# Kernel optimization log

Measured on AMD Instinct MI355X. Metric: run time of the kernel, lower is better.

## Reference

```python
import jax, jax.numpy as jnp
import numpy as np

D_MODEL = 1024
N_HEADS = 16
D_KV = 64
INNER = N_HEADS * D_KV
NUM_BUCKETS = 32
MAX_DISTANCE = 128
B, S = 4, 2048


def _relative_position_bucket(relative_position):
    # Mirrors T5Attention._relative_position_bucket (bidirectional variant)
    num_buckets = NUM_BUCKETS // 2  # 16
    relative_buckets = (relative_position > 0).astype(jnp.int32) * num_buckets
    rp = jnp.abs(relative_position)
    max_exact = num_buckets // 2  # 8
    is_small = rp < max_exact
    # clamp to 1 before log to avoid -inf (masked out by where anyway)
    rp_large = max_exact + (
        jnp.log(jnp.maximum(rp, 1).astype(jnp.float32) / max_exact)
        / np.log(MAX_DISTANCE / max_exact)
        * (num_buckets - max_exact)
    ).astype(jnp.int32)
    rp_large = jnp.minimum(rp_large, num_buckets - 1)
    return relative_buckets + jnp.where(is_small, rp.astype(jnp.int32), rp_large)


def setup_inputs() -> dict:
    key = jax.random.key(0)
    k1, k2, k3, k4, k5, k6 = jax.random.split(key, 6)
    hidden_states = jax.random.normal(k1, (B, S, D_MODEL), dtype=jnp.float32)
    positions = jnp.arange(B * S, dtype=jnp.int64 if jax.config.jax_enable_x64 else jnp.int32).reshape(B, S)
    mask = jnp.ones((B, S), dtype=jnp.float32)
    sc = 1.0 / np.sqrt(D_MODEL)
    wq = jax.random.normal(k2, (INNER, D_MODEL), dtype=jnp.float32) * sc
    wk = jax.random.normal(k3, (INNER, D_MODEL), dtype=jnp.float32) * sc
    wv = jax.random.normal(k4, (INNER, D_MODEL), dtype=jnp.float32) * sc
    wo = jax.random.normal(k5, (D_MODEL, INNER), dtype=jnp.float32) * sc
    rel_bias = jax.random.normal(k6, (NUM_BUCKETS, N_HEADS), dtype=jnp.float32)
    return {"hidden_states": hidden_states, "positions": positions, "mask": mask,
            "wq": wq, "wk": wk, "wv": wv, "wo": wo, "rel_bias": rel_bias}


def reference(hidden_states, positions, mask, wq, wk, wv, wo, rel_bias):
    Bq, Sq, _ = hidden_states.shape

    def shape_heads(x):  # [B,S,inner] -> [B,H,S,dkv]
        return x.reshape(Bq, Sq, N_HEADS, D_KV).transpose(0, 2, 1, 3)

    # position bias: [B,H,Sq,Sk]
    rel_pos = positions[:, None, :] - positions[:, :, None]  # memory - context
    buckets = _relative_position_bucket(rel_pos)             # [B,Sq,Sk]
    position_bias = rel_bias[buckets].transpose(0, 3, 1, 2)  # [B,H,Sq,Sk]

    q = shape_heads(hidden_states @ wq.T).astype(jnp.float32)
    k = shape_heads(hidden_states @ wk.T).astype(jnp.float32)
    v = shape_heads(hidden_states @ wv.T).astype(jnp.float32)

    scores = jnp.einsum('bhqd,bhkd->bhqk', q, k)  # no 1/sqrt(d) scaling (T5)
    bias = position_bias - 1000.0 * (1.0 - mask[:, None, None, :])
    attn = jax.nn.softmax(scores + bias, axis=-1)  # dropout p=0

    ctx = jnp.einsum('bhqk,bhkd->bhqd', attn, v)
    ctx = ctx.transpose(0, 2, 1, 3).reshape(Bq, Sq, INNER).astype(hidden_states.dtype)
    return ctx @ wo.T
```

## Files before the change

kernel.cpp:

```cpp
#include <hip/hip_runtime.h>
#include <cstdint>
#include <cstddef>

#define D_MODEL 1024
#define N_HEADS 16
#define INNER   1024
#define NBATCH  4
#define SEQ     2048
#define MTOT    (NBATCH * SEQ)
#define LOG2E   1.44269504088896f
#define BSTRIDE 4352
#define MASKC   1442.695041f

typedef _Float16 f16;
typedef __attribute__((ext_vector_type(8))) _Float16 f16x8;
typedef __attribute__((ext_vector_type(4))) _Float16 f16x4;
typedef __attribute__((ext_vector_type(2))) _Float16 f16x2;
typedef __attribute__((ext_vector_type(2))) __fp16   h16x2;
typedef __attribute__((ext_vector_type(4))) float    f32x4;

__device__ __forceinline__ f16x2 cvtpk(float x, float y) {
#if __has_builtin(__builtin_amdgcn_cvt_pkrtz)
  h16x2 r = __builtin_amdgcn_cvt_pkrtz(x, y);
  return __builtin_bit_cast(f16x2, r);
#else
  f16x2 r; r[0] = (f16)x; r[1] = (f16)y; return r;
#endif
}
__device__ __forceinline__ float dot2acc(f16x2 p, float acc) {
#if __has_builtin(__builtin_amdgcn_fdot2)
  h16x2 a = __builtin_bit_cast(h16x2, p);
  h16x2 one; one[0] = (__fp16)1.0f; one[1] = (__fp16)1.0f;
  return __builtin_amdgcn_fdot2(a, one, acc, false);
#else
  return acc + (float)p[0] + (float)p[1];
#endif
}

__global__ void k_cvt(const float* __restrict__ src, f16* __restrict__ dst, int n4, float scale) {
  int i = blockIdx.x * 256 + threadIdx.x;
  if (i < n4) {
    const float4 v = reinterpret_cast<const float4*>(src)[i];
    f16x4 h;
    h[0] = (f16)(v.x * scale); h[1] = (f16)(v.y * scale);
    h[2] = (f16)(v.z * scale); h[3] = (f16)(v.w * scale);
    reinterpret_cast<f16x4*>(dst)[i] = h;
  }
}

__global__ void k_cvtw(const float* __restrict__ wq, const float* __restrict__ wk,
                       const float* __restrict__ wv, const float* __restrict__ wo,
                       f16* __restrict__ dq, f16* __restrict__ dk,
                       f16* __restrict__ dv, f16* __restrict__ dwo) {
  const int y = blockIdx.y;
  const float* src = y == 0 ? wq : (y == 1 ? wk : (y == 2 ? wv : wo));
  f16* dst = y == 0 ? dq : (y == 1 ? dk : (y == 2 ? dv : dwo));
  const float scale = y == 0 ? LOG2E : 1.0f;
  const int i = blockIdx.x * 256 + threadIdx.x;
  const float4 v = reinterpret_cast<const float4*>(src)[i];
  f16x4 h;
  h[0] = (f16)(v.x * scale); h[1] = (f16)(v.y * scale);
  h[2] = (f16)(v.z * scale); h[3] = (f16)(v.w * scale);
  reinterpret_cast<f16x4*>(dst)[i] = h;
}

__global__ void k_bias(const float* __restrict__ relb, float* __restrict__ biasG) {
  const int i = blockIdx.x * 256 + threadIdx.x;
  const int h = blockIdx.y;
  const int d = i - 2048;
  const int sgn = d > 0 ? 16 : 0;
  const int a = d < 0 ? -d : d;
  int bucket;
  if (a < 8) {
    bucket = a;
  } else {
    float t = logf((float)a / 8.0f);
    t = t / 2.772588722239781f;
    t = t * 8.0f;
    int lg = 8 + (int)t;
    bucket = lg < 15 ? lg : 15;
  }
  biasG[h * BSTRIDE + i] = relb[(sgn + bucket) * N_HEADS + h] * LOG2E - MASKC;
}

__device__ __forceinline__ void gload_lds16(const void* g, void* l) {
  __builtin_amdgcn_global_load_lds(
      (const __attribute__((address_space(1))) unsigned int*)g,
      (__attribute__((address_space(3))) unsigned int*)l,
      16, 0, 0);
}

template <int MODE>
__device__ __forceinline__ void gemm_body(const f16* __restrict__ A,
                                          const f16* __restrict__ W,
                                          void* __restrict__ Cp,
                                          int m0, int n0) {
  __shared__ __align__(16) f16 As[128 * 64];
  __shared__ __align__(16) f16 Bs[128 * 64];
  const int t = threadIdx.x;
  const int lane = t & 63;
  const int wid = t >> 6;
  const int wr = wid >> 1;
  const int wc = wid & 1;
  const int g = lane >> 4;
  const int lr = lane & 15;

  f32x4 acc[4][4] = {};
  const char* Ab = (const char*)A;
  const char* Wb = (const char*)W;

  for (int kt = 0; kt < D_MODEL / 64; ++kt) {
    const int k0 = kt * 64;
    __syncthreads();
#pragma unroll
    for (int i = 0; i < 4; ++i) {
      const int idx = i * 256 + t;
      const int row = idx >> 3;
      const int cb  = (idx & 7) * 16;
      gload_lds16(Ab + ((size_t)(m0 + row) * D_MODEL + k0) * 2 + cb, (char*)As + idx * 16);
      gload_lds16(Wb + ((size_t)(n0 + row) * D_MODEL + k0) * 2 + cb, (char*)Bs + idx * 16);
    }
    asm volatile("s_waitcnt vmcnt(0)" ::: "memory");
    __syncthreads();

    f16x8 af[4][2], bf[4][2];
#pragma unroll
    for (int mi = 0; mi < 4; ++mi)
#pragma unroll
      for (int kk = 0; kk < 2; ++kk)
        af[mi][kk] = *(const f16x8*)&As[(wr * 64 + mi * 16 + lr) * 64 + kk * 32 + g * 8];
#pragma unroll
    for (int ni = 0; ni < 4; ++ni)
#pragma unroll
      for (int kk = 0; kk < 2; ++kk)
        bf[ni][kk] = *(const f16x8*)&Bs[(wc * 64 + ni * 16 + lr) * 64 + kk * 32 + g * 8];
#pragma unroll
    for (int kk = 0; kk < 2; ++kk)
#pragma unroll
      for (int mi = 0; mi < 4; ++mi)
#pragma unroll
        for (int ni = 0; ni < 4; ++ni)
          acc[mi][ni] = __builtin_amdgcn_mfma_f32_16x16x32_f16(af[mi][kk], bf[ni][kk], acc[mi][ni], 0, 0, 0);
  }

#pragma unroll
  for (int mi = 0; mi < 4; ++mi)
#pragma unroll
    for (int ni = 0; ni < 4; ++ni) {
      const int n = n0 + wc * 64 + ni * 16 + lr;
      if (MODE == 2) {
        const int mbase = m0 + wr * 64 + mi * 16 + g * 4;
        const int b2 = mbase >> 11, s2 = mbase & (SEQ - 1);
        const int h2 = n >> 6, d2 = n & 63;
        const int sub = ((s2 & 15) >> 2) * 8 + ((s2 >> 4) & 1) * 4;
        f16x4 w;
#pragma unroll
        for (int r = 0; r < 4; ++r) w[r] = (f16)acc[mi][ni][r];
        *(f16x4*)((f16*)Cp + ((size_t)((b2 * 16 + h2) * 64 + d2) * SEQ + (s2 >> 5) * 32 + sub)) = w;
      } else {
#pragma unroll
        for (int r = 0; r < 4; ++r) {
          const int m = m0 + wr * 64 + mi * 16 + g * 4 + r;
          if (MODE == 1)
            ((float*)Cp)[(size_t)m * INNER + n] = acc[mi][ni][r];
          else
            ((f16*)Cp)[(size_t)m * INNER + n] = (f16)acc[mi][ni][r];
        }
      }
    }
}

__global__ __launch_bounds__(256) void k_gemm_qkv(
    const f16* __restrict__ A,
    const f16* __restrict__ Wq, const f16* __restrict__ Wk, const f16* __restrict__ Wv,
    f16* __restrict__ Cq, f16* __restrict__ Ck, f16* __restrict__ Vt) {
  const int bid = (int)blockIdx.x;
  const int X = bid & 7, l = bid >> 3;
  const int zy = X * 24 + (l >> 3);
  const int x = l & 7;
  const int z = zy >> 6, y = zy & 63;
  if (z == 0)      gemm_body<0>(A, Wq, Cq, y * 128, x * 128);
  else if (z == 1) gemm_body<0>(A, Wk, Ck, y * 128, x * 128);
  else             gemm_body<2>(A, Wv, Vt, y * 128, x * 128);
}

__global__ __launch_bounds__(256) void k_gemm_out(
    const f16* __restrict__ A, const f16* __restrict__ W, float* __restrict__ C) {
  const int bid = (int)blockIdx.x;
  const int X = bid & 7, l = bid >> 3;
  const int y = X * 8 + (l >> 3), x = l & 7;
  gemm_body<1>(A, W, C, y * 128, x * 128);
}

__global__ __launch_bounds__(512, 4) void k_attn(
    const f16* __restrict__ Q, const f16* __restrict__ K, const f16* __restrict__ Vt,
    const float* __restrict__ biasG, const float* __restrict__ mask,
    f16* __restrict__ ctx) {
  __shared__ __align__(16) float biasQ[4 * 2308];
  __shared__ __align__(16) f16 Ks[2 * 2048];
  __shared__ __align__(16) f16 Vs[2 * 2048];
  __shared__ int mflag;

  const int nb = (int)blockIdx.x;
  const int v = (nb & 7) * 64 + (nb >> 3);
  const int bh = v >> 3, qc = v & 7;
  const int b = bh >> 4, h = bh & 15;

  const int t = threadIdx.x, lane = t & 63, wid = t >> 6;
  const int g = lane >> 4, lr = lane & 15;
  const int qb = qc * 256;

  const float* maskB = mask + (size_t)b * SEQ;
  {
    const float* bgh = biasG + (size_t)h * BSTRIDE + (1793 - qb);
    for (int idx = t; idx < 4 * 576; idx += 512) {
      const int c = idx / 576, m = idx - c * 576;
      const int src = 4 * m + c;
      float4 w;
      w.x = bgh[src]; w.y = bgh[src + 1]; w.z = bgh[src + 2]; w.w = bgh[src + 3];
      *(float4*)&biasQ[c * 2308 + 4 * m] = w;
    }
  }
  if (t == 0) mflag = 1;
  __syncthreads();
  {
    bool bad = false;
    for (int i = t; i < SEQ; i += 512) bad |= (maskB[i] != 1.0f);
    if (bad) mflag = 0;
  }

  const char* Kg = (const char*)K + ((size_t)(b * SEQ) * INNER + h * 64) * 2;
  const char* Vg = (const char*)Vt + ((size_t)bh * 64) * SEQ * 2;

  const bool isK = t < 256;
  const int ts = t & 255;
  const int krow = ts >> 3, kch = ts & 7;
  const int vrow = ts >> 2, vch = ts & 3;
  const int stsrc = isK ? ((kch * 16) ^ ((krow & 7) << 4))
                        : ((vch * 16) ^ ((vrow & 3) << 4));

  const int qw = qb + wid * 32;

  f16x8 qa[2][2];
#pragma unroll
  for (int hh = 0; hh < 2; ++hh)
#pragma unroll
    for (int kk = 0; kk < 2; ++kk)
      qa[hh][kk] = *(const f16x8*)&Q[(size_t)(b * SEQ + qw + hh * 16 + lr) * INNER + h * 64 + kk * 32 + g * 8];

  int koffs[2][2], voffs[4];
#pragma unroll
  for (int s = 0; s < 2; ++s)
#pragma unroll
    for (int hf = 0; hf < 2; ++hf)
      koffs[s][hf] = (s * 16 + lr) * 128 + ((hf * 64 + g * 16) ^ ((lr & 7) << 4));
#pragma unroll
  for (int dn = 0; dn < 4; ++dn)
    voffs[dn] = (dn * 16 + lr) * 64 + ((g * 16) ^ ((lr & 3) << 4));

  f32x4 o[2][4] = {};
  float mrun[2] = {-__builtin_inff(), -__builtin_inff()};
  float lsum[2] = {0.0f, 0.0f};

  const int jbase = 255 + 4 * g - wid * 32 - lr;
  const int jb2 = jbase - 16;
  const char* bqPtr = (const char*)biasQ
                      + (size_t)((jb2 & 3) * 2308 + ((jb2 >> 2) << 2)) * 4;

  if (isK)
    gload_lds16(Kg + ((size_t)krow * INNER) * 2 + stsrc, (char*)Ks + ts * 16);
  else
    gload_lds16(Vg + ((size_t)vrow * SEQ) * 2 + stsrc,   (char*)Vs + ts * 16);
  asm volatile("s_waitcnt vmcnt(0)" ::: "memory");
  __syncthreads();
  const bool useMask = (mflag == 0);

#define ATTN_ITER(BUF, K0, MK)                                                 \
  {                                                                            \
    float4 mk0 = {}, mk1 = {};                                                 \
    if (MK) {                                                                  \
      mk0 = *(const float4*)(maskB + (K0) + 4 * g);                            \
      mk1 = *(const float4*)(maskB + (K0) + 16 + 4 * g);                       \
    }                                                                          \
    const int k0n_ = ((K0) + 32 < SEQ) ? (K0) + 32 : 0;                        \
    if (isK)                                                                   \
      gload_lds16(Kg + ((size_t)(k0n_ + krow) * INNER) * 2 + stsrc,            \
                  (char*)Ks + ((BUF) ^ 1) * 4096 + ts * 16);                   \
    else                                                                       \
      gload_lds16(Vg + ((size_t)vrow * SEQ + k0n_) * 2 + stsrc,                \
                  (char*)Vs + ((BUF) ^ 1) * 4096 + ts * 16);                   \
    const f32x4 bq0 = *(const f32x4*)(bqPtr + (K0) * 4);                       \
    const f32x4 bq1 = *(const f32x4*)(bqPtr + (K0) * 4 + 64);                  \
    const f32x4 bq2 = *(const f32x4*)(bqPtr + (K0) * 4 + 128);                 \
    f16x8 kf[2][2];                                                            \
    _Pragma("unroll") for (int s = 0; s < 2; ++s)                              \
      _Pragma("unroll") for (int hf = 0; hf < 2; ++hf)                         \
        kf[s][hf] = *(const f16x8*)((const char*)Ks + (BUF) * 4096 + koffs[s][hf]); \
    f16x8 vv[4];                                                               \
    _Pragma("unroll") for (int dn = 0; dn < 4; ++dn)                           \
      vv[dn] = *(const f16x8*)((const char*)Vs + (BUF) * 4096 + voffs[dn]);    \
    f32x4 sg[2][2];                                                            \
    __builtin_amdgcn_s_setprio(1);                                             \
    _Pragma("unroll") for (int hh = 0; hh < 2; ++hh)                           \
      _Pragma("unroll") for (int s = 0; s < 2; ++s) {                          \
        const f32x4 bq = hh ? (s ? bq1 : bq0) : (s ? bq2 : bq1);               \
        f32x4 z;                                                               \
        if (MK) {                                                              \
          const float* mkp = (s == 0) ? (const float*)&mk0 : (const float*)&mk1; \
          _Pragma("unroll") for (int r = 0; r < 4; ++r)                        \
            z[r] = fmaf(mkp[r], MASKC, bq[r]);                                 \
        } else {                                                               \
          z = bq;                                                              \
        }                                                                      \
        z = __builtin_amdgcn_mfma_f32_16x16x32_f16(kf[s][0], qa[hh][0], z, 0, 0, 0); \
        z = __builtin_amdgcn_mfma_f32_16x16x32_f16(kf[s][1], qa[hh][1], z, 0, 0, 0); \
        sg[hh][s] = z;                                                         \
      }                                                                        \
    __builtin_amdgcn_s_setprio(0);                                             \
    float mxA = fmaxf(fmaxf(fmaxf(sg[0][0][0], sg[0][0][1]), fmaxf(sg[0][0][2], sg[0][0][3])), \
                      fmaxf(fmaxf(sg[0][1][0], sg[0][1][1]), fmaxf(sg[0][1][2], sg[0][1][3]))); \
    float mxB = fmaxf(fmaxf(fmaxf(sg[1][0][0], sg[1][0][1]), fmaxf(sg[1][0][2], sg[1][0][3])), \
                      fmaxf(fmaxf(sg[1][1][0], sg[1][1][1]), fmaxf(sg[1][1][2], sg[1][1][3]))); \
    if (__any((mxA > mrun[0] + 11.5415603f) || (mxB > mrun[1] + 11.5415603f))) { \
      mxA = fmaxf(mxA, __shfl_xor(mxA, 16));                                   \
      mxB = fmaxf(mxB, __shfl_xor(mxB, 16));                                   \
      mxA = fmaxf(mxA, __shfl_xor(mxA, 32));                                   \
      mxB = fmaxf(mxB, __shfl_xor(mxB, 32));                                   \
      const float mnA = fmaxf(mrun[0], mxA), mnB = fmaxf(mrun[1], mxB);        \
      const float aA = __builtin_amdgcn_exp2f(mrun[0] - mnA);                  \
      const float aB = __builtin_amdgcn_exp2f(mrun[1] - mnB);                  \
      lsum[0] *= aA; lsum[1] *= aB;                                            \
      _Pragma("unroll") for (int dn = 0; dn < 4; ++dn)                         \
        _Pragma("unroll") for (int r = 0; r < 4; ++r) {                        \
          o[0][dn][r] *= aA; o[1][dn][r] *= aB;                                \
        }                                                                      \
      mrun[0] = mnA; mrun[1] = mnB;                                            \
    }                                                                          \
    f16x8 pfA8, pfB8;                                                          \
    _Pragma("unroll") for (int s = 0; s < 2; ++s) {                            \
      float eA[4], eB[4];                                                      \
      _Pragma("unroll") for (int r = 0; r < 4; ++r) {                          \
        eA[r] = __builtin_amdgcn_exp2f(sg[0][s][r] - mrun[0]);                 \
        eB[r] = __builtin_amdgcn_exp2f(sg[1][s][r] - mrun[1]);                 \
      }                                                                        \
      const f16x2 a0 = cvtpk(eA[0], eA[1]), a1 = cvtpk(eA[2], eA[3]);          \
      const f16x2 b0 = cvtpk(eB[0], eB[1]), b1 = cvtpk(eB[2], eB[3]);          \
      lsum[0] = dot2acc(a0, lsum[0]); lsum[0] = dot2acc(a1, lsum[0]);          \
      lsum[1] = dot2acc(b0, lsum[1]); lsum[1] = dot2acc(b1, lsum[1]);          \
      pfA8[s * 4 + 0] = a0[0]; pfA8[s * 4 + 1] = a0[1];                        \
      pfA8[s * 4 + 2] = a1[0]; pfA8[s * 4 + 3] = a1[1];                        \
      pfB8[s * 4 + 0] = b0[0]; pfB8[s * 4 + 1] = b0[1];                        \
      pfB8[s * 4 + 2] = b1[0]; pfB8[s * 4 + 3] = b1[1];                        \
    }                                                                          \
    __builtin_amdgcn_s_setprio(1);                                             \
    _Pragma("unroll") for (int dn = 0; dn < 4; ++dn) {                         \
      o[0][dn] = __builtin_amdgcn_mfma_f32_16x16x32_f16(vv[dn], pfA8, o[0][dn], 0, 0, 0); \
      o[1][dn] = __builtin_amdgcn_mfma_f32_16x16x32_f16(vv[dn], pfB8, o[1][dn], 0, 0, 0); \
    }                                                                          \
    __builtin_amdgcn_s_setprio(0);                                             \
    asm volatile("s_waitcnt vmcnt(0)" ::: "memory");                           \
    __syncthreads();                                                           \
  }

  if (useMask) {
    for (int k0 = 0; k0 < SEQ; k0 += 64) {
      ATTN_ITER(0, k0, 1)
      ATTN_ITER(1, k0 + 32, 1)
    }
  } else {
    for (int k0 = 0; k0 < SEQ; k0 += 64) {
      ATTN_ITER(0, k0, 0)
      ATTN_ITER(1, k0 + 32, 0)
    }
  }

  lsum[0] += __shfl_xor(lsum[0], 16);
  lsum[1] += __shfl_xor(lsum[1], 16);
  lsum[0] += __shfl_xor(lsum[0], 32);
  lsum[1] += __shfl_xor(lsum[1], 32);

  const float invA = 1.0f / lsum[0], invB = 1.0f / lsum[1];
#pragma unroll
  for (int dn = 0; dn < 4; ++dn) {
    f16x4 wA, wB;
#pragma unroll
    for (int r = 0; r < 4; ++r) {
      wA[r] = (f16)(o[0][dn][r] * invA);
      wB[r] = (f16)(o[1][dn][r] * invB);
    }
    *(f16x4*)&ctx[(size_t)(b * SEQ + qw + lr) * INNER + h * 64 + dn * 16 + 4 * g] = wA;
    *(f16x4*)&ctx[(size_t)(b * SEQ + qw + 16 + lr) * INNER + h * 64 + dn * 16 + 4 * g] = wB;
  }
}

extern "C" void kernel_launch(void* const* d_in, const int* in_sizes, int n_in,
                              void* d_out, int out_size, void* d_ws, size_t ws_size,
                              hipStream_t stream) {
  const float* hs   = (const float*)d_in[0];
  const float* mask = (const float*)d_in[2];
  const float* wq   = (const float*)d_in[3];
  const float* wk   = (const float*)d_in[4];
  const float* wv   = (const float*)d_in[5];
  const float* wo   = (const float*)d_in[6];
  const float* relb = (const float*)d_in[7];

  char* ws = (char*)d_ws;
  const size_t SZ16 = (size_t)MTOT * INNER * 2;
  const size_t WSZ  = (size_t)INNER * D_MODEL * 2;
  f16* hs16 = (f16*)(ws);
  f16* q16  = (f16*)(ws + SZ16);
  f16* k16  = (f16*)(ws + 2 * SZ16);
  f16* vt16 = (f16*)(ws + 3 * SZ16);
  f16* wq16 = (f16*)(ws + 4 * SZ16);
  f16* wk16 = (f16*)(ws + 4 * SZ16 + WSZ);
  f16* wv16 = (f16*)(ws + 4 * SZ16 + 2 * WSZ);
  f16* wo16 = (f16*)(ws + 4 * SZ16 + 3 * WSZ);
  float* biasG = (float*)(ws + 4 * SZ16 + 4 * WSZ);

  k_cvt<<<(MTOT * INNER / 4 + 255) / 256, 256, 0, stream>>>(hs, hs16, MTOT * INNER / 4, 1.0f);
  k_cvtw<<<dim3(INNER * D_MODEL / 4 / 256, 4), 256, 0, stream>>>(
      wq, wk, wv, wo, wq16, wk16, wv16, wo16);

  k_bias<<<dim3(BSTRIDE / 256, N_HEADS), 256, 0, stream>>>(relb, biasG);

  k_gemm_qkv<<<dim3(1536), 256, 0, stream>>>(
      hs16, wq16, wk16, wv16, q16, k16, vt16);

  k_attn<<<dim3(512), 512, 0, stream>>>(
      q16, k16, vt16, biasG, mask, hs16);

  k_gemm_out<<<dim3(512), 256, 0, stream>>>(
      hs16, wo16, (float*)d_out);
}
```

Before: 218.6 us.

## Double K/V tile per barrier and compute softmax row sums via MFMA

```diff
diff --git a/kernel.cpp b/kernel.cpp
--- a/kernel.cpp
+++ b/kernel.cpp
@@ -25,15 +25,6 @@
   return __builtin_bit_cast(f16x2, r);
 #else
   f16x2 r; r[0] = (f16)x; r[1] = (f16)y; return r;
-#endif
-}
-__device__ __forceinline__ float dot2acc(f16x2 p, float acc) {
-#if __has_builtin(__builtin_amdgcn_fdot2)
-  h16x2 a = __builtin_bit_cast(h16x2, p);
-  h16x2 one; one[0] = (__fp16)1.0f; one[1] = (__fp16)1.0f;
-  return __builtin_amdgcn_fdot2(a, one, acc, false);
-#else
-  return acc + (float)p[0] + (float)p[1];
 #endif
 }
 
@@ -197,8 +188,8 @@
     const float* __restrict__ biasG, const float* __restrict__ mask,
     f16* __restrict__ ctx) {
   __shared__ __align__(16) float biasQ[4 * 2308];
-  __shared__ __align__(16) f16 Ks[2 * 2048];
-  __shared__ __align__(16) f16 Vs[2 * 2048];
+  __shared__ __align__(16) f16 Ks[2 * 4096];
+  __shared__ __align__(16) f16 Vs[2 * 4096];
   __shared__ int mflag;
 
   const int nb = (int)blockIdx.x;
@@ -259,46 +250,43 @@
     voffs[dn] = (dn * 16 + lr) * 64 + ((g * 16) ^ ((lr & 3) << 4));
 
   f32x4 o[2][4] = {};
+  f32x4 o_l[2] = {};
   float mrun[2] = {-__builtin_inff(), -__builtin_inff()};
-  float lsum[2] = {0.0f, 0.0f};
+  const f16x8 ones8 = {(f16)1, (f16)1, (f16)1, (f16)1, (f16)1, (f16)1, (f16)1, (f16)1};
 
   const int jbase = 255 + 4 * g - wid * 32 - lr;
   const int jb2 = jbase - 16;
   const char* bqPtr = (const char*)biasQ
                       + (size_t)((jb2 & 3) * 2308 + ((jb2 >> 2) << 2)) * 4;
 
-  if (isK)
-    gload_lds16(Kg + ((size_t)krow * INNER) * 2 + stsrc, (char*)Ks + ts * 16);
-  else
-    gload_lds16(Vg + ((size_t)vrow * SEQ) * 2 + stsrc,   (char*)Vs + ts * 16);
+  if (isK) {
+    gload_lds16(Kg + ((size_t)krow * INNER) * 2 + stsrc,        (char*)Ks + ts * 16);
+    gload_lds16(Kg + ((size_t)(krow + 32) * INNER) * 2 + stsrc, (char*)Ks + 4096 + ts * 16);
+  } else {
+    gload_lds16(Vg + ((size_t)vrow * SEQ) * 2 + stsrc,          (char*)Vs + ts * 16);
+    gload_lds16(Vg + ((size_t)vrow * SEQ + 32) * 2 + stsrc,     (char*)Vs + 4096 + ts * 16);
+  }
   asm volatile("s_waitcnt vmcnt(0)" ::: "memory");
   __syncthreads();
   const bool useMask = (mflag == 0);
 
-#define ATTN_ITER(BUF, K0, MK)                                                 \
+#define ATTN_HALF(BUF, K0, SUB, MK)                                            \
   {                                                                            \
     float4 mk0 = {}, mk1 = {};                                                 \
     if (MK) {                                                                  \
       mk0 = *(const float4*)(maskB + (K0) + 4 * g);                            \
       mk1 = *(const float4*)(maskB + (K0) + 16 + 4 * g);                       \
     }                                                                          \
-    const int k0n_ = ((K0) + 32 < SEQ) ? (K0) + 32 : 0;                        \
-    if (isK)                                                                   \
-      gload_lds16(Kg + ((size_t)(k0n_ + krow) * INNER) * 2 + stsrc,            \
-                  (char*)Ks + ((BUF) ^ 1) * 4096 + ts * 16);                   \
-    else                                                                       \
-      gload_lds16(Vg + ((size_t)vrow * SEQ + k0n_) * 2 + stsrc,                \
-                  (char*)Vs + ((BUF) ^ 1) * 4096 + ts * 16);                   \
     const f32x4 bq0 = *(const f32x4*)(bqPtr + (K0) * 4);                       \
     const f32x4 bq1 = *(const f32x4*)(bqPtr + (K0) * 4 + 64);                  \
     const f32x4 bq2 = *(const f32x4*)(bqPtr + (K0) * 4 + 128);                 \
     f16x8 kf[2][2];                                                            \
     _Pragma("unroll") for (int s = 0; s < 2; ++s)                              \
       _Pragma("unroll") for (int hf = 0; hf < 2; ++hf)                         \
-        kf[s][hf] = *(const f16x8*)((const char*)Ks + (BUF) * 4096 + koffs[s][hf]); \
+        kf[s][hf] = *(const f16x8*)((const char*)Ks + (BUF) * 8192 + (SUB) + koffs[s][hf]); \
     f16x8 vv[4];                                                               \
     _Pragma("unroll") for (int dn = 0; dn < 4; ++dn)                           \
-      vv[dn] = *(const f16x8*)((const char*)Vs + (BUF) * 4096 + voffs[dn]);    \
+      vv[dn] = *(const f16x8*)((const char*)Vs + (BUF) * 8192 + (SUB) + voffs[dn]); \
     f32x4 sg[2][2];                                                            \
     __builtin_amdgcn_s_setprio(1);                                             \
     _Pragma("unroll") for (int hh = 0; hh < 2; ++hh)                           \
@@ -329,7 +317,9 @@
       const float mnA = fmaxf(mrun[0], mxA), mnB = fmaxf(mrun[1], mxB);        \
       const float aA = __builtin_amdgcn_exp2f(mrun[0] - mnA);                  \
       const float aB = __builtin_amdgcn_exp2f(mrun[1] - mnB);                  \
-      lsum[0] *= aA; lsum[1] *= aB;                                            \
+      _Pragma("unroll") for (int r = 0; r < 4; ++r) {                          \
+        o_l[0][r] *= aA; o_l[1][r] *= aB;                                      \
+      }                                                                        \
       _Pragma("unroll") for (int dn = 0; dn < 4; ++dn)                         \
         _Pragma("unroll") for (int r = 0; r < 4; ++r) {                        \
           o[0][dn][r] *= aA; o[1][dn][r] *= aB;                                \
@@ -345,8 +335,6 @@
       }                                                                        \
       const f16x2 a0 = cvtpk(eA[0], eA[1]), a1 = cvtpk(eA[2], eA[3]);          \
       const f16x2 b0 = cvtpk(eB[0], eB[1]), b1 = cvtpk(eB[2], eB[3]);          \
-      lsum[0] = dot2acc(a0, lsum[0]); lsum[0] = dot2acc(a1, lsum[0]);          \
-      lsum[1] = dot2acc(b0, lsum[1]); lsum[1] = dot2acc(b1, lsum[1]);          \
       pfA8[s * 4 + 0] = a0[0]; pfA8[s * 4 + 1] = a0[1];                        \
       pfA8[s * 4 + 2] = a1[0]; pfA8[s * 4 + 3] = a1[1];                        \
       pfB8[s * 4 + 0] = b0[0]; pfB8[s * 4 + 1] = b0[1];                        \
@@ -357,29 +345,44 @@
       o[0][dn] = __builtin_amdgcn_mfma_f32_16x16x32_f16(vv[dn], pfA8, o[0][dn], 0, 0, 0); \
       o[1][dn] = __builtin_amdgcn_mfma_f32_16x16x32_f16(vv[dn], pfB8, o[1][dn], 0, 0, 0); \
     }                                                                          \
+    o_l[0] = __builtin_amdgcn_mfma_f32_16x16x32_f16(ones8, pfA8, o_l[0], 0, 0, 0); \
+    o_l[1] = __builtin_amdgcn_mfma_f32_16x16x32_f16(ones8, pfB8, o_l[1], 0, 0, 0); \
     __builtin_amdgcn_s_setprio(0);                                             \
+  }
+
+#define ATTN_ITER(BUF, K0, MK)                                                 \
+  {                                                                            \
+    const int k0n_ = ((K0) + 64 < SEQ) ? (K0) + 64 : 0;                        \
+    if (isK) {                                                                 \
+      gload_lds16(Kg + ((size_t)(k0n_ + krow) * INNER) * 2 + stsrc,            \
+                  (char*)Ks + ((BUF) ^ 1) * 8192 + ts * 16);                   \
+      gload_lds16(Kg + ((size_t)(k0n_ + krow + 32) * INNER) * 2 + stsrc,       \
+                  (char*)Ks + ((BUF) ^ 1) * 8192 + 4096 + ts * 16);            \
+    } else {                                                                   \
+      gload_lds16(Vg + ((size_t)vrow * SEQ + k0n_) * 2 + stsrc,                \
+                  (char*)Vs + ((BUF) ^ 1) * 8192 + ts * 16);                   \
+      gload_lds16(Vg + ((size_t)vrow * SEQ + k0n_ + 32) * 2 + stsrc,           \
+                  (char*)Vs + ((BUF) ^ 1) * 8192 + 4096 + ts * 16);            \
+    }                                                                          \
+    ATTN_HALF(BUF, K0, 0, MK)                                                  \
+    ATTN_HALF(BUF, (K0) + 32, 4096, MK)                                        \
     asm volatile("s_waitcnt vmcnt(0)" ::: "memory");                           \
     __syncthreads();                                                           \
   }
 
   if (useMask) {
-    for (int k0 = 0; k0 < SEQ; k0 += 64) {
+    for (int k0 = 0; k0 < SEQ; k0 += 128) {
       ATTN_ITER(0, k0, 1)
-      ATTN_ITER(1, k0 + 32, 1)
+      ATTN_ITER(1, k0 + 64, 1)
     }
   } else {
-    for (int k0 = 0; k0 < SEQ; k0 += 64) {
+    for (int k0 = 0; k0 < SEQ; k0 += 128) {
       ATTN_ITER(0, k0, 0)
-      ATTN_ITER(1, k0 + 32, 0)
-    }
-  }
-
-  lsum[0] += __shfl_xor(lsum[0], 16);
-  lsum[1] += __shfl_xor(lsum[1], 16);
-  lsum[0] += __shfl_xor(lsum[0], 32);
-  lsum[1] += __shfl_xor(lsum[1], 32);
-
-  const float invA = 1.0f / lsum[0], invB = 1.0f / lsum[1];
+      ATTN_ITER(1, k0 + 64, 0)
+    }
+  }
+
+  const float invA = 1.0f / o_l[0][0], invB = 1.0f / o_l[1][0];
 #pragma unroll
   for (int dn = 0; dn < 4; ++dn) {
     f16x4 wA, wB;
```

Result: slower. 282.8 us (+29.3%).
